# Performance work log

Measured on AMD Instinct MI355X. Metric: run time of the kernel, lower is better.

## Reference

```python
import jax, jax.numpy as jnp
import numpy as np

COMMITMENT_COST = 0.25
N_EMBED = 1024
EMB_DIM = 256

def setup_inputs() -> dict:
    key = jax.random.key(0)
    k1, k2 = jax.random.split(key)
    z = jax.random.normal(k1, (32, EMB_DIM, 32, 32), dtype=jnp.float32)
    # embedding.weight.data.uniform_(-1/n_embed, 1/n_embed)
    embedding = jax.random.uniform(k2, (N_EMBED, EMB_DIM), dtype=jnp.float32,
                                   minval=-1.0 / N_EMBED, maxval=1.0 / N_EMBED)
    return {"z": z, "embedding": embedding}

def reference(z, embedding):
    # NCHW -> NHWC
    zp = jnp.transpose(z, (0, 2, 3, 1))            # [B,H,W,D]
    in_shape = zp.shape
    flat = zp.reshape(-1, in_shape[-1])            # [N,D]
    # squared L2 distances (argmin equivalent to p=2 cdist argmin)
    d2 = (jnp.sum(flat * flat, axis=1, keepdims=True)
          - 2.0 * (flat @ embedding.T)
          + jnp.sum(embedding * embedding, axis=1))  # [N,K]
    idx = jnp.argmin(d2, axis=1)                   # [N]
    # one-hot @ codebook == direct gather
    z_quant = embedding[idx].reshape(in_shape)     # [B,H,W,D]
    codebook_loss = jnp.mean((z_quant - jax.lax.stop_gradient(zp)) ** 2)
    commitment_loss = jnp.mean((zp - jax.lax.stop_gradient(z_quant)) ** 2)
    loss = codebook_loss + COMMITMENT_COST * commitment_loss
    # straight-through estimator
    z_st = zp + jax.lax.stop_gradient(z_quant - zp)
    z_st = jnp.transpose(z_st, (0, 3, 1, 2))       # NHWC -> NCHW
    return (z_st, loss, codebook_loss, commitment_loss)
```

## Files before the change

kernel.cpp:

```cpp
#include <hip/hip_runtime.h>
#include <hip/hip_bf16.h>
#include <stdint.h>


typedef short v8s __attribute__((ext_vector_type(8)));
typedef float v4f __attribute__((ext_vector_type(4)));

__device__ inline unsigned short f2bf(float f) {
    uint32_t u = __float_as_uint(f);
    return (unsigned short)((u + 0x7fffu + ((u >> 16) & 1u)) >> 16);
}

__global__ __launch_bounds__(512) void k_prep_a(const float* __restrict__ z,
                                                unsigned short* __restrict__ Abf) {
    int tid = threadIdx.x;
    int b = blockIdx.x >> 4, hw0 = (blockIdx.x & 15) << 6;
    int t15 = tid & 15, dblk = tid >> 4;
    const float* zp = z + ((size_t)b << 18) + (size_t)(dblk << 3) * 1024 + hw0 + (t15 << 2);
    float4 L[8];
#pragma unroll
    for (int j = 0; j < 8; j++)
        L[j] = *(const float4*)(zp + (size_t)j * 1024);
    const float* Lf = (const float*)L;
    v8s* Aout = (v8s*)Abf + ((size_t)(b * 1024 + hw0 + (t15 << 2))) * 32 + dblk;
#pragma unroll
    for (int c = 0; c < 4; c++) {
        union { v8s v; unsigned short s[8]; } u;
#pragma unroll
        for (int j = 0; j < 8; j++) u.s[j] = f2bf(Lf[j * 4 + c]);
        Aout[(size_t)c * 32] = u.v;
    }
}

__global__ __launch_bounds__(256) void k_prep_e(const float* __restrict__ E,
                                                unsigned short* __restrict__ Ebf,
                                                float* __restrict__ nE,
                                                float* __restrict__ accum) {
    int k = blockIdx.x, tid = threadIdx.x;
    float v = E[(size_t)k * 256 + tid];
    Ebf[(size_t)k * 256 + tid] = f2bf(v);
    float s = v * v;
#pragma unroll
    for (int off = 1; off < 64; off <<= 1) s += __shfl_xor(s, off);
    __shared__ float w4[4];
    if ((tid & 63) == 0) w4[tid >> 6] = s;
    __syncthreads();
    if (tid == 0) {
        nE[k] = 0.5f * (w4[0] + w4[1] + w4[2] + w4[3]);
        if (k == 0) accum[0] = 0.f;
    }
}

__global__ __launch_bounds__(256, 2) void k_main(
        const unsigned short* __restrict__ Abf,
        const unsigned short* __restrict__ Ebf,
        const float* __restrict__ nE,
        const float* __restrict__ z,
        const float* __restrict__ E,
        float* __restrict__ out,
        float* __restrict__ accum) {
    __shared__ union {
        v8s   B[2][2048];
        float Eg[32][260];
    } S;
    __shared__ int   idxLds[64];
    __shared__ float w4[4];

    int tid = threadIdx.x;
    int lane = tid & 63, w = tid >> 6;
    int g = lane >> 4, m = lane & 15;
    int R0 = blockIdx.x << 6;
    int b = R0 >> 10, hw0 = R0 & 1023;

    v8s a[8];
    {
        const v8s* Ap = (const v8s*)Abf;
        int row = R0 + w * 16 + m;
#pragma unroll
        for (int dc = 0; dc < 8; dc++)
            a[dc] = Ap[(size_t)row * 32 + dc * 4 + g];
    }

    const v8s* Ep = (const v8s*)Ebf;
#define STAGE(ch, bufSel)                                                     \
    {                                                                         \
        _Pragma("unroll")                                                     \
        for (int k = 0; k < 8; k++) {                                         \
            int u  = (((w << 3) + k) << 6) + lane;                            \
            int um = u & 15, ug = (u >> 4) & 3;                               \
            int udc = (u >> 6) & 7, uct = (u >> 9) & 3;                       \
            const v8s* gp = Ep + ((size_t)((ch) * 64 + uct * 16 + um) * 32    \
                                  + udc * 4 + ug);                            \
            __builtin_amdgcn_global_load_lds(                                 \
                (const __attribute__((address_space(1))) void*)gp,            \
                (__attribute__((address_space(3))) void*)                     \
                    &S.B[bufSel][((w << 3) + k) << 6],                        \
                16, 0, 0);                                                    \
        }                                                                     \
    }

    float best[4]; int bidx[4];
#pragma unroll
    for (int r = 0; r < 4; r++) { best[r] = 3.4e38f; bidx[r] = 0; }

    STAGE(0, 0);
#pragma unroll 1
    for (int ct = 0; ct < 16; ct++) {
        int cur = ct & 1;
        __syncthreads();
        if (ct < 15) STAGE(ct + 1, cur ^ 1);
        float ne4[4];
#pragma unroll
        for (int t = 0; t < 4; t++) ne4[t] = nE[ct * 64 + t * 16 + m];
#pragma unroll
        for (int t = 0; t < 4; t++) {
            v4f acc = {0.f, 0.f, 0.f, 0.f};
#pragma unroll
            for (int dc = 0; dc < 8; dc++) {
                v8s bf = S.B[cur][t * 512 + dc * 64 + g * 16 + m];
                acc = __builtin_amdgcn_mfma_f32_16x16x32_bf16(a[dc], bf, acc, 0, 0, 0);
            }
            int code = ct * 64 + t * 16 + m;
#pragma unroll
            for (int r = 0; r < 4; r++) {
                float s = ne4[t] - acc[r];
                if (s < best[r]) { best[r] = s; bidx[r] = code; }
            }
        }
    }

#pragma unroll
    for (int r = 0; r < 4; r++) {
        uint32_t sb = __float_as_uint(best[r]);
        sb = (sb & 0x80000000u) ? ~sb : (sb | 0x80000000u);
        unsigned long long pk = ((unsigned long long)sb << 32) | (uint32_t)bidx[r];
#pragma unroll
        for (int off = 1; off < 16; off <<= 1) {
            unsigned long long o = __shfl_xor(pk, off);
            if (o < pk) pk = o;
        }
        if (m == 0)
            idxLds[w * 16 + g * 4 + r] = (int)(pk & 0xffffffffu);
    }
    __syncthreads();

    float lsum = 0.f;
    const float* zb = z + ((size_t)b << 18);
    float* ob = out + ((size_t)b << 18);
#pragma unroll 1
    for (int h = 0; h < 2; h++) {
        {
            int j2 = tid >> 3, dq = tid & 7;
            int k = idxLds[h * 32 + j2];
            const float* ep = E + (size_t)k * 256 + (dq << 2);
#pragma unroll
            for (int i = 0; i < 8; i++)
                *(float4*)&S.Eg[j2][(dq << 2) + i * 32] =
                    *(const float4*)(ep + i * 32);
        }
        __syncthreads();
        {
            int jj = (tid & 7) << 2, dt = tid >> 3;
#pragma unroll
            for (int i = 0; i < 8; i++) {
                int d = dt + (i << 5);
                size_t o = (size_t)d * 1024 + hw0 + (h << 5) + jj;
                float4 zv = *(const float4*)(zb + o);
                float4 ev;
                ev.x = S.Eg[jj + 0][d]; ev.y = S.Eg[jj + 1][d];
                ev.z = S.Eg[jj + 2][d]; ev.w = S.Eg[jj + 3][d];
                *(float4*)(ob + o) = ev;
                float dx = ev.x - zv.x, dy = ev.y - zv.y;
                float dz2 = ev.z - zv.z, dw = ev.w - zv.w;
                lsum += dx * dx + dy * dy + dz2 * dz2 + dw * dw;
            }
        }
        __syncthreads();
    }
#pragma unroll
    for (int off = 1; off < 64; off <<= 1) lsum += __shfl_xor(lsum, off);
    if ((tid & 63) == 0) w4[tid >> 6] = lsum;
    __syncthreads();
    if (tid == 0) atomicAdd(accum, w4[0] + w4[1] + w4[2] + w4[3]);
#undef STAGE
}

__global__ void k_loss(const float* __restrict__ accum, float* __restrict__ out) {
    if (threadIdx.x == 0) {
        float s = accum[0] * (1.0f / 8388608.0f);
        out[8388608] = 1.25f * s;
        out[8388609] = s;
        out[8388610] = s;
    }
}

extern "C" void kernel_launch(void* const* d_in, const int* in_sizes, int n_in,
                              void* d_out, int out_size, void* d_ws, size_t ws_size,
                              hipStream_t stream) {
    const float* z = (const float*)d_in[0];
    const float* E = (const float*)d_in[1];
    char* ws = (char*)d_ws;
    unsigned short* Abf   = (unsigned short*)(ws);
    unsigned short* Ebf   = (unsigned short*)(ws + 16777216);
    float*          nE    = (float*)(ws + 17301504);
    float*          accum = (float*)(ws + 17305600);
    float* out = (float*)d_out;

    hipLaunchKernelGGL(k_prep_e, dim3(1024), dim3(256), 0, stream, E, Ebf, nE, accum);
    hipLaunchKernelGGL(k_prep_a, dim3(512),  dim3(512), 0, stream, z, Abf);
    hipLaunchKernelGGL(k_main,   dim3(512),  dim3(256), 0, stream,
                       Abf, Ebf, nE, z, E, out, accum);
    hipLaunchKernelGGL(k_loss,   dim3(1),    dim3(64),  0, stream, accum, out);
}
```

Measured before the change: 141.0 us.

## Double rows per block, pre-swizzle codebook, cache norms in LDS

Each k_main block now handles 128 rows instead of 64, so every staged codebook tile is reused by two A fragments per wave. This halves the global-to-LDS codebook traffic per row and halves the grid to 256 blocks. k_prep_e now writes the bf16 codebook already in MFMA fragment order, so staging becomes contiguous loads. Codebook norms are also cached in LDS and the gather/writeback loop is restructured. The cost is fewer blocks (256 on a large GPU), with a risk of under-occupancy, plus higher register pressure from the doubled accumulators.

Result: faster. 131.1 us (-7.0%).

```diff
diff --git a/kernel.cpp b/kernel.cpp
--- a/kernel.cpp
+++ b/kernel.cpp
@@ -33,27 +33,44 @@
 }
 
 __global__ __launch_bounds__(256) void k_prep_e(const float* __restrict__ E,
-                                                unsigned short* __restrict__ Ebf,
+                                                v8s* __restrict__ Esw,
                                                 float* __restrict__ nE,
                                                 float* __restrict__ accum) {
-    int k = blockIdx.x, tid = threadIdx.x;
-    float v = E[(size_t)k * 256 + tid];
-    Ebf[(size_t)k * 256 + tid] = f2bf(v);
-    float s = v * v;
-#pragma unroll
-    for (int off = 1; off < 64; off <<= 1) s += __shfl_xor(s, off);
-    __shared__ float w4[4];
-    if ((tid & 63) == 0) w4[tid >> 6] = s;
+    __shared__ float Ef[16][264];
+    int q = blockIdx.x, tid = threadIdx.x;
+    const float4* Ein = (const float4*)(E + ((size_t)q << 12));
+#pragma unroll
+    for (int i = 0; i < 4; i++) {
+        int f4 = i * 256 + tid;
+        int row = f4 >> 6, c4 = (f4 & 63) << 2;
+        *(float4*)&Ef[row][c4] = Ein[f4];
+    }
     __syncthreads();
-    if (tid == 0) {
-        nE[k] = 0.5f * (w4[0] + w4[1] + w4[2] + w4[3]);
-        if (k == 0) accum[0] = 0.f;
-    }
-}
-
-__global__ __launch_bounds__(256, 2) void k_main(
+    {
+        int c = tid >> 4, l = tid & 15;
+        float s = 0.f;
+#pragma unroll
+        for (int j = 0; j < 16; j++) { float v = Ef[c][l + 16 * j]; s += v * v; }
+#pragma unroll
+        for (int off = 1; off < 16; off <<= 1) s += __shfl_xor(s, off);
+        if (l == 0) nE[q * 16 + c] = 0.5f * s;
+    }
+#pragma unroll
+    for (int i = 0; i < 2; i++) {
+        int u = tid + i * 256;
+        int um = u & 15, ug = (u >> 4) & 3, udc = (u >> 6) & 7;
+        int d0 = udc * 32 + ug * 8;
+        union { v8s v; unsigned short s[8]; } pk;
+#pragma unroll
+        for (int e = 0; e < 8; e++) pk.s[e] = f2bf(Ef[um][d0 + e]);
+        Esw[((size_t)q << 9) + u] = pk.v;
+    }
+    if (q == 0 && tid == 0) accum[0] = 0.f;
+}
+
+__global__ __launch_bounds__(256) void k_main(
         const unsigned short* __restrict__ Abf,
-        const unsigned short* __restrict__ Ebf,
+        const v8s* __restrict__ Esw,
         const float* __restrict__ nE,
         const float* __restrict__ z,
         const float* __restrict__ E,
@@ -61,47 +78,51 @@
         float* __restrict__ accum) {
     __shared__ union {
         v8s   B[2][2048];
-        float Eg[32][260];
+        float Eg[32 * 260];
     } S;
-    __shared__ int   idxLds[64];
+    __shared__ float nEl[1024];
+    __shared__ int   idxLds[128];
     __shared__ float w4[4];
 
     int tid = threadIdx.x;
     int lane = tid & 63, w = tid >> 6;
     int g = lane >> 4, m = lane & 15;
-    int R0 = blockIdx.x << 6;
+    int R0 = blockIdx.x << 7;
     int b = R0 >> 10, hw0 = R0 & 1023;
 
-    v8s a[8];
+#pragma unroll
+    for (int i = 0; i < 4; i++) nEl[tid + i * 256] = nE[tid + i * 256];
+
+    v8s a[2][8];
     {
         const v8s* Ap = (const v8s*)Abf;
-        int row = R0 + w * 16 + m;
-#pragma unroll
-        for (int dc = 0; dc < 8; dc++)
-            a[dc] = Ap[(size_t)row * 32 + dc * 4 + g];
-    }
-
-    const v8s* Ep = (const v8s*)Ebf;
-#define STAGE(ch, bufSel)                                                     \
+#pragma unroll
+        for (int s = 0; s < 2; s++) {
+            int row = R0 + w * 32 + s * 16 + m;
+#pragma unroll
+            for (int dc = 0; dc < 8; dc++)
+                a[s][dc] = Ap[(size_t)row * 32 + dc * 4 + g];
+        }
+    }
+
+#define STAGE(ch, buf)                                                        \
     {                                                                         \
         _Pragma("unroll")                                                     \
-        for (int k = 0; k < 8; k++) {                                         \
-            int u  = (((w << 3) + k) << 6) + lane;                            \
-            int um = u & 15, ug = (u >> 4) & 3;                               \
-            int udc = (u >> 6) & 7, uct = (u >> 9) & 3;                       \
-            const v8s* gp = Ep + ((size_t)((ch) * 64 + uct * 16 + um) * 32    \
-                                  + udc * 4 + ug);                            \
+        for (int j = 0; j < 8; j++) {                                         \
             __builtin_amdgcn_global_load_lds(                                 \
-                (const __attribute__((address_space(1))) void*)gp,            \
+                (const __attribute__((address_space(1))) void*)               \
+                    (Esw + ((size_t)(ch) << 11) + (j << 8) + tid),            \
                 (__attribute__((address_space(3))) void*)                     \
-                    &S.B[bufSel][((w << 3) + k) << 6],                        \
+                    &S.B[buf][(j << 8) + (w << 6)],                           \
                 16, 0, 0);                                                    \
         }                                                                     \
     }
 
-    float best[4]; int bidx[4];
-#pragma unroll
-    for (int r = 0; r < 4; r++) { best[r] = 3.4e38f; bidx[r] = 0; }
+    float best[2][4]; int bidx[2][4];
+#pragma unroll
+    for (int s = 0; s < 2; s++)
+#pragma unroll
+        for (int r = 0; r < 4; r++) { best[s][r] = 3.4e38f; bidx[s][r] = 0; }
 
     STAGE(0, 0);
 #pragma unroll 1
@@ -109,77 +130,84 @@
         int cur = ct & 1;
         __syncthreads();
         if (ct < 15) STAGE(ct + 1, cur ^ 1);
-        float ne4[4];
-#pragma unroll
-        for (int t = 0; t < 4; t++) ne4[t] = nE[ct * 64 + t * 16 + m];
+        float ne[4];
+#pragma unroll
+        for (int t = 0; t < 4; t++) ne[t] = nEl[(ct << 6) + t * 16 + m];
+        v4f acc[4][2];
+#pragma unroll
+        for (int t = 0; t < 4; t++)
+#pragma unroll
+            for (int s = 0; s < 2; s++) acc[t][s] = (v4f){0.f, 0.f, 0.f, 0.f};
+#pragma unroll
+        for (int dc = 0; dc < 8; dc++) {
+#pragma unroll
+            for (int t = 0; t < 4; t++) {
+                v8s bf = S.B[cur][t * 512 + dc * 64 + g * 16 + m];
+                acc[t][0] = __builtin_amdgcn_mfma_f32_16x16x32_bf16(a[0][dc], bf, acc[t][0], 0, 0, 0);
+                acc[t][1] = __builtin_amdgcn_mfma_f32_16x16x32_bf16(a[1][dc], bf, acc[t][1], 0, 0, 0);
+            }
+        }
 #pragma unroll
         for (int t = 0; t < 4; t++) {
-            v4f acc = {0.f, 0.f, 0.f, 0.f};
-#pragma unroll
-            for (int dc = 0; dc < 8; dc++) {
-                v8s bf = S.B[cur][t * 512 + dc * 64 + g * 16 + m];
-                acc = __builtin_amdgcn_mfma_f32_16x16x32_bf16(a[dc], bf, acc, 0, 0, 0);
+            int code = (ct << 6) + t * 16 + m;
+#pragma unroll
+            for (int r = 0; r < 4; r++) {
+                float s0 = ne[t] - acc[t][0][r];
+                if (s0 < best[0][r]) { best[0][r] = s0; bidx[0][r] = code; }
+                float s1 = ne[t] - acc[t][1][r];
+                if (s1 < best[1][r]) { best[1][r] = s1; bidx[1][r] = code; }
             }
-            int code = ct * 64 + t * 16 + m;
-#pragma unroll
-            for (int r = 0; r < 4; r++) {
-                float s = ne4[t] - acc[r];
-                if (s < best[r]) { best[r] = s; bidx[r] = code; }
+        }
+    }
+
+#pragma unroll
+    for (int s = 0; s < 2; s++)
+#pragma unroll
+        for (int r = 0; r < 4; r++) {
+            uint32_t sb = __float_as_uint(best[s][r]);
+            sb = (sb & 0x80000000u) ? ~sb : (sb | 0x80000000u);
+            unsigned long long pk = ((unsigned long long)sb << 32) | (uint32_t)bidx[s][r];
+#pragma unroll
+            for (int off = 1; off < 16; off <<= 1) {
+                unsigned long long o = __shfl_xor(pk, off);
+                if (o < pk) pk = o;
             }
-        }
-    }
-
-#pragma unroll
-    for (int r = 0; r < 4; r++) {
-        uint32_t sb = __float_as_uint(best[r]);
-        sb = (sb & 0x80000000u) ? ~sb : (sb | 0x80000000u);
-        unsigned long long pk = ((unsigned long long)sb << 32) | (uint32_t)bidx[r];
-#pragma unroll
-        for (int off = 1; off < 16; off <<= 1) {
-            unsigned long long o = __shfl_xor(pk, off);
-            if (o < pk) pk = o;
-        }
-        if (m == 0)
-            idxLds[w * 16 + g * 4 + r] = (int)(pk & 0xffffffffu);
-    }
-    __syncthreads();
+            if (m == 0)
+                idxLds[w * 32 + s * 16 + g * 4 + r] = (int)(pk & 0xffffffffu);
+        }
 
     float lsum = 0.f;
     const float* zb = z + ((size_t)b << 18);
     float* ob = out + ((size_t)b << 18);
+    int jj = (tid & 7) << 2, dt = tid >> 3;
 #pragma unroll 1
-    for (int h = 0; h < 2; h++) {
-        {
-            int j2 = tid >> 3, dq = tid & 7;
-            int k = idxLds[h * 32 + j2];
-            const float* ep = E + (size_t)k * 256 + (dq << 2);
-#pragma unroll
-            for (int i = 0; i < 8; i++)
-                *(float4*)&S.Eg[j2][(dq << 2) + i * 32] =
-                    *(const float4*)(ep + i * 32);
-        }
+    for (int h = 0; h < 4; h++) {
         __syncthreads();
-        {
-            int jj = (tid & 7) << 2, dt = tid >> 3;
-#pragma unroll
-            for (int i = 0; i < 8; i++) {
-                int d = dt + (i << 5);
-                size_t o = (size_t)d * 1024 + hw0 + (h << 5) + jj;
-                float4 zv = *(const float4*)(zb + o);
-                float4 ev;
-                ev.x = S.Eg[jj + 0][d]; ev.y = S.Eg[jj + 1][d];
-                ev.z = S.Eg[jj + 2][d]; ev.w = S.Eg[jj + 3][d];
-                *(float4*)(ob + o) = ev;
-                float dx = ev.x - zv.x, dy = ev.y - zv.y;
-                float dz2 = ev.z - zv.z, dw = ev.w - zv.w;
-                lsum += dx * dx + dy * dy + dz2 * dz2 + dw * dw;
-            }
+#pragma unroll
+        for (int i = 0; i < 8; i++) {
+            int row = w + (i << 2);
+            int k = idxLds[(h << 5) + row];
+            float4 v = ((const float4*)(E + ((size_t)k << 8)))[lane];
+            *(float4*)&S.Eg[row * 260 + (lane << 2)] = v;
         }
         __syncthreads();
+#pragma unroll
+        for (int i = 0; i < 8; i++) {
+            int d = dt + (i << 5);
+            size_t o = (size_t)d * 1024 + hw0 + (h << 5) + jj;
+            float4 zv = *(const float4*)(zb + o);
+            float4 ev;
+            ev.x = S.Eg[(jj + 0) * 260 + d]; ev.y = S.Eg[(jj + 1) * 260 + d];
+            ev.z = S.Eg[(jj + 2) * 260 + d]; ev.w = S.Eg[(jj + 3) * 260 + d];
+            *(float4*)(ob + o) = ev;
+            float dx = ev.x - zv.x, dy = ev.y - zv.y;
+            float dz2 = ev.z - zv.z, dw = ev.w - zv.w;
+            lsum += dx * dx + dy * dy + dz2 * dz2 + dw * dw;
+        }
     }
 #pragma unroll
     for (int off = 1; off < 64; off <<= 1) lsum += __shfl_xor(lsum, off);
-    if ((tid & 63) == 0) w4[tid >> 6] = lsum;
+    if ((tid & 63) == 0) w4[w] = lsum;
     __syncthreads();
     if (tid == 0) atomicAdd(accum, w4[0] + w4[1] + w4[2] + w4[3]);
 #undef STAGE
@@ -201,14 +229,14 @@
     const float* E = (const float*)d_in[1];
     char* ws = (char*)d_ws;
     unsigned short* Abf   = (unsigned short*)(ws);
-    unsigned short* Ebf   = (unsigned short*)(ws + 16777216);
+    v8s*            Esw   = (v8s*)(ws + 16777216);
     float*          nE    = (float*)(ws + 17301504);
     float*          accum = (float*)(ws + 17305600);
     float* out = (float*)d_out;
 
-    hipLaunchKernelGGL(k_prep_e, dim3(1024), dim3(256), 0, stream, E, Ebf, nE, accum);
-    hipLaunchKernelGGL(k_prep_a, dim3(512),  dim3(512), 0, stream, z, Abf);
-    hipLaunchKernelGGL(k_main,   dim3(512),  dim3(256), 0, stream,
-                       Abf, Ebf, nE, z, E, out, accum);
-    hipLaunchKernelGGL(k_loss,   dim3(1),    dim3(64),  0, stream, accum, out);
-}
+    hipLaunchKernelGGL(k_prep_e, dim3(64),  dim3(256), 0, stream, E, Esw, nE, accum);
+    hipLaunchKernelGGL(k_prep_a, dim3(512), dim3(512), 0, stream, z, Abf);
+    hipLaunchKernelGGL(k_main,   dim3(256), dim3(256), 0, stream,
+                       Abf, Esw, nE, z, E, out, accum);
+    hipLaunchKernelGGL(k_loss,   dim3(1),   dim3(64),  0, stream, accum, out);
+}
```
